# Kernel tuning notes

Hardware: AMD Instinct MI355X
Metric: run time of the kernel (lower is better)

Reference implementation:

```python
import jax, jax.numpy as jnp
import numpy as np

N, E, DN, DE, H, L = 2048, 32768, 512, 512, 8, 2
BN_EPS = 1e-5  # torch BatchNorm1d eps; eval mode with running_mean=0, running_var=1


def setup_inputs():
    key = jax.random.key(0)
    ks = jax.random.split(key, 12)
    rng = np.random.default_rng(0)
    # unique directed edges: 3E/4 upper-triangular pairs + reverses of the first E/4
    iu, ju = np.triu_indices(N, k=1)
    sel = rng.choice(iu.size, size=3 * E // 4, replace=False)
    s, d = iu[sel], ju[sel]
    src = np.concatenate([s, d[: E // 4]])
    dst = np.concatenate([d, s[: E // 4]])
    edge_index = jnp.asarray(np.stack([src, dst]).astype(np.int32))

    def p(k, shape, fan_in):
        return jax.random.normal(k, shape, jnp.float32) / np.sqrt(fan_in).astype(np.float32)

    return dict(
        x=jax.random.normal(ks[0], (N, DN), jnp.float32),
        edge_feature=jax.random.normal(ks[1], (E, DE), jnp.float32),
        node_pos=jax.random.uniform(ks[2], (N, 3), jnp.float32) * 10.0,
        inw=p(ks[3], (L, 3 * DN, DN), DN),          # MHA in_proj_weight per layer
        inb=jnp.zeros((L, 3 * DN), jnp.float32),
        ow=p(ks[4], (L, DN, DN), DN),               # MHA out_proj
        ob=jnp.zeros((L, DN), jnp.float32),
        etw=p(ks[5], (L, DE, DE), DE),              # edge_transform Linear
        etb=jnp.zeros((L, DE), jnp.float32),
        etg=jnp.ones((L, DE), jnp.float32),         # edge_transform BN gamma
        etbb=jnp.zeros((L, DE), jnp.float32),       # edge_transform BN beta
        unw=p(ks[6], (L, DN, DN + DE), DN + DE),    # update_node Linear
        unb=jnp.zeros((L, DN), jnp.float32),
        uew=p(ks[7], (L, DE, 2 * DN + 2 * DE), 2 * DN + 2 * DE),  # update_edge Linear
        ueb=jnp.zeros((L, DE), jnp.float32),
        edge_index=edge_index,
    )


def _forward(x, edge_feature, node_pos, inw, inb, ow, ob, etw, etb, etg, etbb, unw, unb, uew, ueb, edge_index):
    src, dst = edge_index[0], edge_index[1]
    n, e = x.shape[0], src.shape[0]
    hd = DN // H
    # vectorized reverse-edge lookup (mirrors the torch edge_dict)
    keys = src * n + dst
    rkeys = dst * n + src
    order = jnp.argsort(keys)
    sk = keys[order]
    pos = jnp.clip(jnp.searchsorted(sk, rkeys), 0, e - 1)
    found = sk[pos] == rkeys
    rev_idx = order[pos]
    # distance-based attention mask: -inf everywhere, 1/(dist+eps) on (symmetric) edges, 1.0 on diagonal
    diff = node_pos[src] - node_pos[dst]
    w = 1.0 / (jnp.sqrt(jnp.sum(diff * diff, axis=-1)) + 1e-6)
    mask = jnp.full((n, n), -jnp.inf, x.dtype)
    mask = mask.at[src, dst].set(w).at[dst, src].set(w)
    diag = jnp.arange(n)
    mask = mask.at[diag, diag].set(1.0)
    bn_scale = np.float32(1.0 / np.sqrt(1.0 + BN_EPS))
    nf, ef = x, edge_feature
    for l in range(L):
        rev = jnp.where(found[:, None], ef[rev_idx], 0.0)
        # MHSA over all nodes as one sequence (batch=1), eval mode (dropout off)
        qkv = nf @ inw[l].T + inb[l]
        q, k, v = [t.reshape(n, H, hd) for t in jnp.split(qkv, 3, axis=-1)]
        scores = jnp.einsum('nhd,mhd->hnm', q * np.float32(1.0 / np.sqrt(hd)), k) + mask
        attn = jax.nn.softmax(scores, axis=-1)
        ctx = jnp.einsum('hnm,mhd->nhd', attn, v).reshape(n, DN)
        x_upd = ctx @ ow[l].T + ob[l]
        # message: update_edge on [x_i, e, e_rev, x_j] (flow=target_to_source -> x_i = x[src])
        upd_edge = jnp.concatenate([nf[src], ef, rev, nf[dst]], axis=1) @ uew[l].T + ueb[l]
        # edge_transform = Linear + BN(eval) + ReLU
        te = jax.nn.relu((ef @ etw[l].T + etb[l]) * bn_scale * etg[l] + etbb[l])
        # scatter-max to subject/object nodes (empty segments -> 0, torch_scatter convention)
        subj = jax.ops.segment_max(te, src, num_segments=n)
        obj = jax.ops.segment_max(te, dst, num_segments=n)
        subj = jnp.where(jnp.isneginf(subj), 0.0, subj)
        obj = jnp.where(jnp.isneginf(obj), 0.0, obj)
        nf = jnp.concatenate([x_upd, subj + obj], axis=1) @ unw[l].T + unb[l]
        ef = upd_edge
        if l < L - 1 or L == 1:
            nf = jax.nn.relu(nf)
            ef = jax.nn.relu(ef)
    return nf, ef


def reference(x, edge_feature, node_pos, inw, inb, ow, ob, etw, etb, etg, etbb, unw, unb, uew, ueb, edge_index):
    return _forward(x, edge_feature, node_pos, inw, inb, ow, ob, etw, etb, etg, etbb, unw, unb, uew, ueb, edge_index)
```

## Files before the change

kernel.cpp:

```cpp
#include <hip/hip_runtime.h>
#include <hip/hip_bf16.h>

#define NN 2048
#define EE 32768
#define DND 512
#define NH 8
#define HD 64
#define MAXD 128
#define NEGF (-1e30f)
#define BN_SCALE 0.9999950000374997f

typedef __attribute__((ext_vector_type(8))) short bf16x8;
typedef __attribute__((ext_vector_type(4))) float f32x4;
typedef unsigned short u16;
typedef unsigned int u32;

static __device__ __forceinline__ float4 ld4(const float* p) {
    return *reinterpret_cast<const float4*>(p);
}
static __device__ __forceinline__ u16 f2b(float f) {
    __hip_bfloat16 h = __float2bfloat16(f);
    return *reinterpret_cast<u16*>(&h);
}
static __device__ __forceinline__ float b2f(u32 bits) {
    return __uint_as_float(bits << 16);
}
static __device__ __forceinline__ void gl_lds(const u16* g, u16* l) {
    __builtin_amdgcn_global_load_lds((const __attribute__((address_space(1))) void*)g,
                                     (__attribute__((address_space(3))) void*)l, 16, 0, 0);
}


__global__ __launch_bounds__(256) void setup_init_k(u32* __restrict__ t2,
                                                    int* __restrict__ adj, float* __restrict__ wadj,
                                                    int* __restrict__ cnt,
                                                    int* __restrict__ ocnt, int* __restrict__ icnt,
                                                    u16* __restrict__ zero)
{
    int i = blockIdx.x * 256 + threadIdx.x;
    t2[i] = 0xFFFFFFFFu;
    if (i < NN) {
        cnt[i] = 1; adj[i * MAXD] = i; wadj[i * MAXD] = 1.0f;
        ocnt[i] = 0; icnt[i] = 0;
    }
    if (i < 1024) zero[i] = 0;
}

__global__ __launch_bounds__(256) void fill_scatter_k(const int* __restrict__ ei, u16* __restrict__ t,
                                                      int* __restrict__ oadj, int* __restrict__ ocnt,
                                                      int* __restrict__ iadj, int* __restrict__ icnt)
{
    int e = blockIdx.x * 256 + threadIdx.x;
    if (e >= EE) return;
    int s = ei[e], d = ei[EE + e];
    t[(size_t)s * NN + d] = (u16)e;
    int slot = atomicAdd(&ocnt[s], 1);
    if (slot < MAXD) oadj[s * MAXD + slot] = e;
    slot = atomicAdd(&icnt[d], 1);
    if (slot < MAXD) iadj[d * MAXD + slot] = e;
}

__global__ __launch_bounds__(256) void rev_csr_k(const int* __restrict__ ei, const u16* __restrict__ t,
                                                 const float* __restrict__ pos,
                                                 int* __restrict__ rev,
                                                 int* __restrict__ adj, float* __restrict__ wadj,
                                                 int* __restrict__ cnt)
{
    int e = blockIdx.x * 256 + threadIdx.x;
    if (e >= EE) return;
    int s = ei[e], d = ei[EE + e];
    u16 r16 = t[(size_t)d * NN + s];
    int r = (r16 == 0xFFFFu) ? -1 : (int)r16;
    rev[e] = r;
    float dx = pos[s * 3 + 0] - pos[d * 3 + 0];
    float dy = pos[s * 3 + 1] - pos[d * 3 + 1];
    float dz = pos[s * 3 + 2] - pos[d * 3 + 2];
    float w = 1.0f / (sqrtf(dx * dx + dy * dy + dz * dz) + 1e-6f);
    int slot = atomicAdd(&cnt[s], 1);
    if (slot < MAXD) { adj[s * MAXD + slot] = d; wadj[s * MAXD + slot] = w; }
    if (r < 0) {
        slot = atomicAdd(&cnt[d], 1);
        if (slot < MAXD) { adj[d * MAXD + slot] = s; wadj[d * MAXD + slot] = w; }
    }
}

__global__ __launch_bounds__(256) void conv_all_k(
    const float* __restrict__ x, const float* __restrict__ inw, const float* __restrict__ ow,
    const float* __restrict__ etw, const float* __restrict__ unw, const float* __restrict__ uew,
    const float* __restrict__ efin, u16* __restrict__ dst)
{
    size_t i = ((size_t)blockIdx.x * 256 + threadIdx.x) * 8;
    const float* s;
    size_t off;
    if (i < 1048576)      { s = x;    off = i; }
    else if (i < 2621440) { s = inw;  off = i - 1048576; }
    else if (i < 3145728) { s = ow;   off = i - 2621440; }
    else if (i < 3670016) { s = etw;  off = i - 3145728; }
    else if (i < 4718592) { s = unw;  off = i - 3670016; }
    else if (i < 6815744) { s = uew;  off = i - 4718592; }
    else                  { s = efin; off = i - 6815744; }
    float4 a = ld4(s + off), b = ld4(s + off + 4);
    u16 o[8];
    o[0] = f2b(a.x); o[1] = f2b(a.y); o[2] = f2b(a.z); o[3] = f2b(a.w);
    o[4] = f2b(b.x); o[5] = f2b(b.y); o[6] = f2b(b.z); o[7] = f2b(b.w);
    *reinterpret_cast<int4*>(dst + i) = *reinterpret_cast<const int4*>(o);
}

__global__ __launch_bounds__(256) void gather_max_k(const u16* __restrict__ te,
                                                    const int* __restrict__ oadj, const int* __restrict__ ocnt,
                                                    const int* __restrict__ iadj, const int* __restrict__ icnt,
                                                    u16* __restrict__ sums)
{
    const int i = blockIdx.x;
    const int c2 = threadIdx.x;
    float ms0 = 0.f, ms1 = 0.f, mo0 = 0.f, mo1 = 0.f;
    int no = ocnt[i]; if (no > MAXD) no = MAXD;
    for (int s = 0; s < no; ++s) {
        const int e = oadj[i * MAXD + s];
        const u32 v = *reinterpret_cast<const u32*>(te + (size_t)e * DND + c2 * 2);
        ms0 = fmaxf(ms0, b2f(v & 0xffffu));
        ms1 = fmaxf(ms1, b2f(v >> 16));
    }
    int ni = icnt[i]; if (ni > MAXD) ni = MAXD;
    for (int s = 0; s < ni; ++s) {
        const int e = iadj[i * MAXD + s];
        const u32 v = *reinterpret_cast<const u32*>(te + (size_t)e * DND + c2 * 2);
        mo0 = fmaxf(mo0, b2f(v & 0xffffu));
        mo1 = fmaxf(mo1, b2f(v >> 16));
    }
    const u32 r = (u32)f2b(ms0 + mo0) | ((u32)f2b(ms1 + mo1) << 16);
    *reinterpret_cast<u32*>(sums + (size_t)i * DND + c2 * 2) = r;
}

template <int MODE, int EPI, int WF32, int WBF16, int GY>
__global__ __launch_bounds__(256) void mgemm_k(
    const u16* __restrict__ WS, u32 a_off, u32 b_off, const float* __restrict__ bias,
    float* __restrict__ Cf, u16* __restrict__ Cb, int M, int Nc, int K,
    u32 g0_off, u32 g1_off, u32 gz_off,
    const int* __restrict__ srcv, const int* __restrict__ dstv, const int* __restrict__ revv,
    const float* __restrict__ eg, const float* __restrict__ eb)
{
    __shared__ u16 As2[2][8192];
    __shared__ u16 Bs2[2][8192];
    const int tid = threadIdx.x, lane = tid & 63, w = tid >> 6;
    const int wr = w >> 1, wc = w & 1;
    const int b = blockIdx.x;
    const int xcd = b & 7, kb = b >> 3;
    const int bm = ((kb / GY) * 8 + xcd) * 128;
    const int bn = (kb % GY) * 128;

    const int rl = lane >> 3;
    const u32 lx = (u32)(((lane & 7) ^ rl) * 8);

    u32 offA0[4], offA1[4], offB[4];
#pragma unroll
    for (int q = 0; q < 4; ++q) {
        const int ra = bm + w * 32 + q * 8 + rl;
        if (MODE == 0) {
            offA0[q] = a_off + (u32)ra * (u32)K + lx;
        } else {
            offA0[q] = g0_off + (u32)ra * 512u + lx;
            offA1[q] = g1_off + (u32)ra * 512u + lx;
        }
        offB[q] = b_off + (u32)(bn + w * 32 + q * 8 + rl) * (u32)K + lx;
    }

    const int nks = K >> 6;
    const int kq = lane >> 4, li = lane & 15;

    auto stage = [&](int t, int buf) {
        const u32 k0 = (u32)t * 64u;
        const int seg = (MODE == 0) ? 0 : (int)(k0 >> 9);
#pragma unroll
        for (int q = 0; q < 4; ++q) {
            u32 oa = (MODE == 0) ? offA0[q] : (seg == 0 ? offA0[q] : offA1[q]);
            const u32 koff = (MODE == 0) ? k0 : (k0 & 511u);
            gl_lds(WS + oa + koff, &As2[buf][(w * 32 + q * 8) * 64]);
        }
#pragma unroll
        for (int q = 0; q < 4; ++q)
            gl_lds(WS + offB[q] + k0, &Bs2[buf][(w * 32 + q * 8) * 64]);
    };

    f32x4 acc[4][4] = {};
    const int baseA = (wr * 64 + li) * 64 + ((kq ^ (li & 7)) * 8);
    const int baseB = (wc * 64 + li) * 64 + ((kq ^ (li & 7)) * 8);

    stage(0, 0);
    for (int t = 0; t < nks; ++t) {
        const int cur = t & 1;
        if (t + 1 < nks) stage(t + 1, cur ^ 1);
        if (t + 1 < nks) asm volatile("s_waitcnt vmcnt(8)" ::: "memory");
        else             asm volatile("s_waitcnt vmcnt(0)" ::: "memory");
        __builtin_amdgcn_s_barrier();
        __builtin_amdgcn_sched_barrier(0);
#pragma unroll
        for (int sub = 0; sub < 2; ++sub) {
            const int sx = sub << 5;
            bf16x8 af[4], bf[4];
#pragma unroll
            for (int m = 0; m < 4; ++m)
                af[m] = *reinterpret_cast<const bf16x8*>(&As2[cur][(baseA + m * 1024) ^ sx]);
#pragma unroll
            for (int n = 0; n < 4; ++n)
                bf[n] = *reinterpret_cast<const bf16x8*>(&Bs2[cur][(baseB + n * 1024) ^ sx]);
#pragma unroll
            for (int m = 0; m < 4; ++m)
#pragma unroll
                for (int n = 0; n < 4; ++n)
                    acc[m][n] = __builtin_amdgcn_mfma_f32_16x16x32_bf16(af[m], bf[n], acc[m][n], 0, 0, 0);
        }
        __builtin_amdgcn_s_barrier();
        __builtin_amdgcn_sched_barrier(0);
    }

    float bsv[4], scv[4], shv[4];
#pragma unroll
    for (int n = 0; n < 4; ++n) {
        const int col = bn + wc * 64 + n * 16 + li;
        bsv[n] = bias[col];
        if (EPI == 2) { scv[n] = BN_SCALE * eg[col]; shv[n] = eb[col]; }
    }
#pragma unroll
    for (int m = 0; m < 4; ++m) {
#pragma unroll
        for (int n = 0; n < 4; ++n) {
            const int col = bn + wc * 64 + n * 16 + li;
#pragma unroll
            for (int i = 0; i < 4; ++i) {
                float v = acc[m][n][i] + bsv[n];
                if (EPI == 2) v = fmaxf(fmaf(v, scv[n], shv[n]), 0.f);
                else if (EPI == 1) v = fmaxf(v, 0.f);
                const int r = bm + wr * 64 + m * 16 + (lane >> 4) * 4 + i;
                if (WF32) Cf[(size_t)r * Nc + col] = v;
                if (WBF16) Cb[(size_t)r * Nc + col] = f2b(v);
            }
        }
    }
}

template <int MODE, int EPI, int WF32, int WBF16>
__global__ __launch_bounds__(512, 2) void mgemm256_k(
    const u16* __restrict__ WS, u32 a_off, u32 b_off, const float* __restrict__ bias,
    float* __restrict__ Cf, u16* __restrict__ Cb, int M, int Nc, int K,
    u32 g0_off, u32 g1_off, u32 gz_off,
    const int* __restrict__ srcv, const int* __restrict__ dstv, const int* __restrict__ revv,
    const float* __restrict__ eg, const float* __restrict__ eb)
{
    __shared__ u16 SB[65536];
    const int tid = threadIdx.x, lane = tid & 63, w = tid >> 6;
    const int wr = w >> 2, wc = w & 3;
    const int b = blockIdx.x;
    const int bm = ((b & 7) + 8 * (b >> 4)) * 256;
    const int bn = ((b >> 3) & 1) * 256;

    const int rl = lane >> 3;
    const u32 lx = (u32)(((lane & 7) ^ rl) * 8);

    u32 offA0[4], offA1[4], offA2[4], offA3[4], offB[4];
#pragma unroll
    for (int q = 0; q < 4; ++q) {
        const int ra = bm + w * 32 + q * 8 + rl;
        if (MODE == 0) {
            offA0[q] = a_off + (u32)ra * (u32)K + lx;
        } else {
            offA0[q] = g0_off + (u32)srcv[ra] * 512u + lx;
            offA1[q] = g1_off + (u32)ra * 512u + lx;
            const int rv = revv[ra];
            offA2[q] = (rv >= 0 ? g1_off + (u32)rv * 512u : gz_off) + lx;
            offA3[q] = g0_off + (u32)dstv[ra] * 512u + lx;
        }
        offB[q] = b_off + (u32)(bn + w * 32 + q * 8 + rl) * (u32)K + lx;
    }

    const int nks = K >> 6;
    const int kq = lane >> 4, li = lane & 15;

    auto stageA2 = [&](int t, int buf, int q0) {
        const u32 k0 = (u32)t * 64u;
        const int seg = (MODE == 0) ? 0 : (int)(k0 >> 9);
        const u32 koff = (MODE == 0) ? k0 : (k0 & 511u);
#pragma unroll
        for (int q = q0; q < q0 + 2; ++q) {
            u32 oa;
            if (MODE == 0) oa = offA0[q];
            else           oa = (seg == 0 ? offA0[q] : seg == 1 ? offA1[q] : seg == 2 ? offA2[q] : offA3[q]);
            gl_lds(WS + oa + koff, &SB[buf * 16384 + (w * 32 + q * 8) * 64]);
        }
    };
    auto stageB2 = [&](int t, int buf, int q0) {
        const u32 k0 = (u32)t * 64u;
#pragma unroll
        for (int q = q0; q < q0 + 2; ++q)
            gl_lds(WS + offB[q] + k0, &SB[32768 + buf * 16384 + (w * 32 + q * 8) * 64]);
    };

    f32x4 acc[8][4] = {};
    const int baseA = (wr * 128 + li) * 64 + ((kq ^ (li & 7)) * 8);
    const int baseB = (wc * 64 + li) * 64 + ((kq ^ (li & 7)) * 8);

    stageA2(0, 0, 0); stageA2(0, 0, 2); stageB2(0, 0, 0); stageB2(0, 0, 2);
    for (int t = 0; t < nks; ++t) {
        const int cur = t & 1;
        const bool pf = (t + 1 < nks);
        if (pf) {
            stageA2(t + 1, cur ^ 1, 0);
            asm volatile("s_waitcnt vmcnt(2)" ::: "memory");
        } else {
            asm volatile("s_waitcnt vmcnt(0)" ::: "memory");
        }
        __builtin_amdgcn_s_barrier();
        __builtin_amdgcn_sched_barrier(0);
#pragma unroll
        for (int sub = 0; sub < 2; ++sub) {
            const int sx = sub << 5;
            bf16x8 bf[4];
#pragma unroll
            for (int n = 0; n < 4; ++n)
                bf[n] = *reinterpret_cast<const bf16x8*>(&SB[(32768 + cur * 16384 + baseB + n * 1024) ^ sx]);
#pragma unroll
            for (int mh = 0; mh < 2; ++mh) {
                if (pf) {
                    if (sub == 0 && mh == 0)      stageA2(t + 1, cur ^ 1, 2);
                    else if (sub == 0 && mh == 1) stageB2(t + 1, cur ^ 1, 0);
                    else if (sub == 1 && mh == 0) stageB2(t + 1, cur ^ 1, 2);
                }
                bf16x8 af[4];
#pragma unroll
                for (int m = 0; m < 4; ++m)
                    af[m] = *reinterpret_cast<const bf16x8*>(&SB[(cur * 16384 + baseA + (mh * 4 + m) * 1024) ^ sx]);
                __builtin_amdgcn_sched_barrier(0);
                __builtin_amdgcn_s_setprio(1);
#pragma unroll
                for (int m = 0; m < 4; ++m)
#pragma unroll
                    for (int n = 0; n < 4; ++n)
                        acc[mh * 4 + m][n] =
                            __builtin_amdgcn_mfma_f32_16x16x32_bf16(af[m], bf[n], acc[mh * 4 + m][n], 0, 0, 0);
                __builtin_amdgcn_s_setprio(0);
                __builtin_amdgcn_sched_barrier(0);
            }
        }
        __builtin_amdgcn_s_barrier();
        __builtin_amdgcn_sched_barrier(0);
    }

    float bsv[4], scv[4], shv[4];
#pragma unroll
    for (int n = 0; n < 4; ++n) {
        const int col = bn + wc * 64 + n * 16 + li;
        bsv[n] = bias[col];
        if (EPI == 2) { scv[n] = BN_SCALE * eg[col]; shv[n] = eb[col]; }
    }
#pragma unroll
    for (int m = 0; m < 8; ++m) {
#pragma unroll
        for (int n = 0; n < 4; ++n) {
            const int col = bn + wc * 64 + n * 16 + li;
#pragma unroll
            for (int i = 0; i < 4; ++i) {
                float v = acc[m][n][i] + bsv[n];
                if (EPI == 2) v = fmaxf(fmaf(v, scv[n], shv[n]), 0.f);
                else if (EPI == 1) v = fmaxf(v, 0.f);
                const int r = bm + wr * 128 + m * 16 + (lane >> 4) * 4 + i;
                if (WF32) Cf[(size_t)r * Nc + col] = v;
                if (WBF16) Cb[(size_t)r * Nc + col] = f2b(v);
            }
        }
    }
}

__global__ __launch_bounds__(256) void attn_sp_k(const u16* __restrict__ qkvb,
                                                 const int* __restrict__ adj,
                                                 const float* __restrict__ wadj,
                                                 const int* __restrict__ cnt,
                                                 u16* __restrict__ ctxb)
{
    const int i = blockIdx.x;
    const int wv = threadIdx.x >> 6, lane = threadIdx.x & 63;
    const int h = blockIdx.y * 4 + wv;
    __shared__ float qs[4][64];
    qs[wv][lane] = b2f((u32)qkvb[(size_t)i * 1536 + h * HD + lane]) * 0.125f;
    __syncthreads();
    int deg = cnt[i];
    if (deg > MAXD) deg = MAXD;
    float m = -3.0e38f, lsum = 0.f, c = 0.f;
    for (int base = 0; base < deg; base += 64) {
        int nn_ = deg - base; if (nn_ > 64) nn_ = 64;
        int j = 0;
        float s = NEGF;
        if (lane < nn_) {
            j = adj[i * MAXD + base + lane];
            const float wgt = wadj[i * MAXD + base + lane];
            const u16* kr = qkvb + (size_t)j * 1536 + DND + h * HD;
            float accd = 0.f;
#pragma unroll
            for (int cq = 0; cq < 4; ++cq) {
                uint4 kv = *reinterpret_cast<const uint4*>(kr + cq * 16);
                const float* qp = &qs[wv][cq * 16];
                accd = fmaf(qp[0],  b2f(kv.x & 0xffffu), accd);
                accd = fmaf(qp[1],  b2f(kv.x >> 16), accd);
                accd = fmaf(qp[2],  b2f(kv.y & 0xffffu), accd);
                accd = fmaf(qp[3],  b2f(kv.y >> 16), accd);
                accd = fmaf(qp[4],  b2f(kv.z & 0xffffu), accd);
                accd = fmaf(qp[5],  b2f(kv.z >> 16), accd);
                accd = fmaf(qp[6],  b2f(kv.w & 0xffffu), accd);
                accd = fmaf(qp[7],  b2f(kv.w >> 16), accd);
                uint4 kv2 = *reinterpret_cast<const uint4*>(kr + cq * 16 + 8);
                accd = fmaf(qp[8],  b2f(kv2.x & 0xffffu), accd);
                accd = fmaf(qp[9],  b2f(kv2.x >> 16), accd);
                accd = fmaf(qp[10], b2f(kv2.y & 0xffffu), accd);
                accd = fmaf(qp[11], b2f(kv2.y >> 16), accd);
                accd = fmaf(qp[12], b2f(kv2.z & 0xffffu), accd);
                accd = fmaf(qp[13], b2f(kv2.z >> 16), accd);
                accd = fmaf(qp[14], b2f(kv2.w & 0xffffu), accd);
                accd = fmaf(qp[15], b2f(kv2.w >> 16), accd);
            }
            s = accd + wgt;
        }
        float mloc = s;
#pragma unroll
        for (int o = 1; o < 64; o <<= 1) mloc = fmaxf(mloc, __shfl_xor(mloc, o, 64));
        const float mnew = fmaxf(m, mloc);
        const float alpha = __expf(m - mnew);
        const float p = (lane < nn_) ? __expf(s - mnew) : 0.f;
        float ps = p;
#pragma unroll
        for (int o = 1; o < 64; o <<= 1) ps += __shfl_xor(ps, o, 64);
        lsum = lsum * alpha + ps;
        c *= alpha;
        for (int l = 0; l < nn_; ++l) {
            const float pj = __shfl(p, l, 64);
            const int jj = __shfl(j, l, 64);
            c = fmaf(pj, b2f((u32)qkvb[(size_t)jj * 1536 + 2 * DND + h * HD + lane]), c);
        }
        m = mnew;
    }
    ctxb[(size_t)i * DND + h * HD + lane] = f2b(c / lsum);
}

extern "C" void kernel_launch(void* const* d_in, const int* in_sizes, int n_in,
                              void* d_out, int out_size, void* d_ws, size_t ws_size,
                              hipStream_t stream)
{
    const float* x    = (const float*)d_in[0];
    const float* efin = (const float*)d_in[1];
    const float* pos  = (const float*)d_in[2];
    const float* inw  = (const float*)d_in[3];
    const float* inb  = (const float*)d_in[4];
    const float* ow   = (const float*)d_in[5];
    const float* ob   = (const float*)d_in[6];
    const float* etw  = (const float*)d_in[7];
    const float* etb  = (const float*)d_in[8];
    const float* etg  = (const float*)d_in[9];
    const float* etbb = (const float*)d_in[10];
    const float* unw  = (const float*)d_in[11];
    const float* unb  = (const float*)d_in[12];
    const float* uew  = (const float*)d_in[13];
    const float* ueb  = (const float*)d_in[14];
    const int*   ei   = (const int*)d_in[15];

    float* W = (float*)d_ws;
    u16*   qkvb  = (u16*)W;
    u16*   te    = (u16*)W;
    int*   rev   = (int*)(W + 8388608);
    u16*   zero  = (u16*)(W + 8421376);
    int*   adj   = (int*)(W + 8421888);
    float* wadj  = W + 8684032;
    int*   cnt   = (int*)(W + 8946176);
    int*   oadj  = (int*)(W + 8948224);
    int*   ocnt  = (int*)(W + 9210368);
    int*   iadj  = (int*)(W + 9212416);
    int*   icnt  = (int*)(W + 9474560);
    u16*   ctxb  = (u16*)(W + 9476608);
    u16*   xupdb = (u16*)(W + 10000896);
    u16*   sums  = (u16*)(W + 10525184);
    u16*   nfb   = (u16*)(W + 11049472);
    u16*   wbf   = (u16*)(W + 11573760);
    u16*   efbA  = (u16*)(W + 14457344);
    u16*   efbB  = (u16*)(W + 22845952);
    u16*   table = (u16*)efbA;

    u16* inwb = wbf;
    u16* owb  = wbf + 1572864;
    u16* etwb = wbf + 2097152;
    u16* unwb = wbf + 2621440;
    u16* uewb = wbf + 3670016;

    float* out_nf = (float*)d_out;
    float* out_ef = out_nf + (size_t)NN * DND;

    const int* srcv = ei;
    const int* dstv = ei + EE;

    const u16* WSu = (const u16*)d_ws;
    auto uoff = [&](const void* p) { return (u32)((const u16*)p - WSu); };

    setup_init_k<<<NN * NN / 512, 256, 0, stream>>>((u32*)table, adj, wadj, cnt, ocnt, icnt, zero);
    fill_scatter_k<<<EE / 256, 256, 0, stream>>>(ei, table, oadj, ocnt, iadj, icnt);
    rev_csr_k<<<EE / 256, 256, 0, stream>>>(ei, table, pos, rev, adj, wadj, cnt);
    conv_all_k<<<11520, 256, 0, stream>>>(x, inw, ow, etw, unw, uew, efin, nfb);

    for (int l = 0; l < 2; ++l) {
        const u16* efb_cur = l ? efbB : efbA;
        const u16* inwb_l = inwb + (size_t)l * 786432;
        const u16* owb_l  = owb  + (size_t)l * 262144;
        const u16* etwb_l = etwb + (size_t)l * 262144;
        const u16* unwb_l = unwb + (size_t)l * 524288;
        const u16* uewb_l = uewb + (size_t)l * 1048576;
        const float* inb_l  = inb  + (size_t)l * 1536;
        const float* ob_l   = ob   + (size_t)l * 512;
        const float* etb_l  = etb  + (size_t)l * 512;
        const float* etg_l  = etg  + (size_t)l * 512;
        const float* etbb_l = etbb + (size_t)l * 512;
        const float* unb_l  = unb  + (size_t)l * 512;
        const float* ueb_l  = ueb  + (size_t)l * 512;

        mgemm_k<0, 0, 0, 1, 12><<<192, 256, 0, stream>>>(
            WSu, uoff(nfb), uoff(inwb_l), inb_l, nullptr, qkvb, NN, 1536, DND,
            0, 0, 0, nullptr, nullptr, nullptr, nullptr, nullptr);

        attn_sp_k<<<dim3(NN, 2), 256, 0, stream>>>(qkvb, adj, wadj, cnt, ctxb);

        mgemm_k<0, 0, 0, 1, 4><<<64, 256, 0, stream>>>(
            WSu, uoff(ctxb), uoff(owb_l), ob_l, nullptr, xupdb, NN, DND, DND,
            0, 0, 0, nullptr, nullptr, nullptr, nullptr, nullptr);

        mgemm256_k<0, 2, 0, 1><<<256, 512, 0, stream>>>(
            WSu, uoff(efb_cur), uoff(etwb_l), etb_l, nullptr, te, EE, DND, DND,
            0, 0, 0, nullptr, nullptr, nullptr, etg_l, etbb_l);

        gather_max_k<<<NN, 256, 0, stream>>>(te, oadj, ocnt, iadj, icnt, sums);

        if (l == 0)
            mgemm256_k<1, 1, 0, 1><<<256, 512, 0, stream>>>(
                WSu, 0, uoff(uewb_l), ueb_l, nullptr, efbB, EE, DND, 2048,
                uoff(nfb), uoff(efb_cur), uoff(zero), srcv, dstv, rev, nullptr, nullptr);
        else
            mgemm256_k<1, 0, 1, 0><<<256, 512, 0, stream>>>(
                WSu, 0, uoff(uewb_l), ueb_l, out_ef, nullptr, EE, DND, 2048,
                uoff(nfb), uoff(efb_cur), uoff(zero), srcv, dstv, rev, nullptr, nullptr);

        if (l == 0)
            mgemm_k<2, 1, 0, 1, 4><<<64, 256, 0, stream>>>(
                WSu, 0, uoff(unwb_l), unb_l, nullptr, nfb, NN, DND, 1024,
                uoff(xupdb), uoff(sums), 0, nullptr, nullptr, nullptr, nullptr, nullptr);
        else
            mgemm_k<2, 0, 1, 0, 4><<<64, 256, 0, stream>>>(
                WSu, 0, uoff(unwb_l), unb_l, out_nf, nullptr, NN, DND, 1024,
                uoff(xupdb), uoff(sums), 0, nullptr, nullptr, nullptr, nullptr, nullptr);
    }
}
```

Measured before the change: 429.8 us.

## Restructure GEMM main loop into four-phase half-tile prefetch pipeline

Reorganizes the 256x256 bf16 MFMA GEMM main loop into four phases per K-step. Each phase loads an A/B quarter from LDS and issues a half-tile global-to-LDS prefetch up to two steps ahead, with staging rows remapped so each half-tile lands in a region that is no longer being read. The goal is to overlap global loads with MFMA work more deeply and to spread barriers across phases. In exchange it adds more barriers per K-step and intricate vmcnt accounting, which risks stalls or races if the counts are wrong.

```diff
diff --git a/kernel.cpp b/kernel.cpp
--- a/kernel.cpp
+++ b/kernel.cpp
@@ -257,92 +257,110 @@
     const int rl = lane >> 3;
     const u32 lx = (u32)(((lane & 7) ^ rl) * 8);
 
+    int arb[4], brb[4];
+#pragma unroll
+    for (int h = 0; h < 2; ++h)
+#pragma unroll
+        for (int q = 0; q < 2; ++q) {
+            arb[h * 2 + q] = (w < 4 ? w * 16 : 128 + (w - 4) * 16) + h * 64 + q * 8;
+            brb[h * 2 + q] = (w >> 1) * 64 + (w & 1) * 16 + h * 32 + q * 8;
+        }
+
     u32 offA0[4], offA1[4], offA2[4], offA3[4], offB[4];
 #pragma unroll
-    for (int q = 0; q < 4; ++q) {
-        const int ra = bm + w * 32 + q * 8 + rl;
+    for (int i = 0; i < 4; ++i) {
+        const int ra = bm + arb[i] + rl;
         if (MODE == 0) {
-            offA0[q] = a_off + (u32)ra * (u32)K + lx;
+            offA0[i] = a_off + (u32)ra * (u32)K + lx;
         } else {
-            offA0[q] = g0_off + (u32)srcv[ra] * 512u + lx;
-            offA1[q] = g1_off + (u32)ra * 512u + lx;
+            offA0[i] = g0_off + (u32)srcv[ra] * 512u + lx;
+            offA1[i] = g1_off + (u32)ra * 512u + lx;
             const int rv = revv[ra];
-            offA2[q] = (rv >= 0 ? g1_off + (u32)rv * 512u : gz_off) + lx;
-            offA3[q] = g0_off + (u32)dstv[ra] * 512u + lx;
-        }
-        offB[q] = b_off + (u32)(bn + w * 32 + q * 8 + rl) * (u32)K + lx;
+            offA2[i] = (rv >= 0 ? g1_off + (u32)rv * 512u : gz_off) + lx;
+            offA3[i] = g0_off + (u32)dstv[ra] * 512u + lx;
+        }
+        offB[i] = b_off + (u32)(bn + brb[i] + rl) * (u32)K + lx;
     }
 
     const int nks = K >> 6;
     const int kq = lane >> 4, li = lane & 15;
 
-    auto stageA2 = [&](int t, int buf, int q0) {
+    auto stageA = [&](int t, int h) {
         const u32 k0 = (u32)t * 64u;
+        const int par = t & 1;
         const int seg = (MODE == 0) ? 0 : (int)(k0 >> 9);
         const u32 koff = (MODE == 0) ? k0 : (k0 & 511u);
 #pragma unroll
-        for (int q = q0; q < q0 + 2; ++q) {
+        for (int q = 0; q < 2; ++q) {
+            const int i = h * 2 + q;
             u32 oa;
-            if (MODE == 0) oa = offA0[q];
-            else           oa = (seg == 0 ? offA0[q] : seg == 1 ? offA1[q] : seg == 2 ? offA2[q] : offA3[q]);
-            gl_lds(WS + oa + koff, &SB[buf * 16384 + (w * 32 + q * 8) * 64]);
+            if (MODE == 0) oa = offA0[i];
+            else           oa = (seg == 0 ? offA0[i] : seg == 1 ? offA1[i] : seg == 2 ? offA2[i] : offA3[i]);
+            gl_lds(WS + oa + koff, &SB[par * 16384 + arb[i] * 64]);
         }
     };
-    auto stageB2 = [&](int t, int buf, int q0) {
+    auto stageB = [&](int t, int h) {
         const u32 k0 = (u32)t * 64u;
-#pragma unroll
-        for (int q = q0; q < q0 + 2; ++q)
-            gl_lds(WS + offB[q] + k0, &SB[32768 + buf * 16384 + (w * 32 + q * 8) * 64]);
+        const int par = t & 1;
+#pragma unroll
+        for (int q = 0; q < 2; ++q) {
+            const int i = h * 2 + q;
+            gl_lds(WS + offB[i] + k0, &SB[32768 + par * 16384 + brb[i] * 64]);
+        }
     };
 
     f32x4 acc[8][4] = {};
-    const int baseA = (wr * 128 + li) * 64 + ((kq ^ (li & 7)) * 8);
-    const int baseB = (wc * 64 + li) * 64 + ((kq ^ (li & 7)) * 8);
-
-    stageA2(0, 0, 0); stageA2(0, 0, 2); stageB2(0, 0, 0); stageB2(0, 0, 2);
+    const u32 swz = (u32)((kq ^ (li & 7)) * 8);
+
+    stageA(0, 0); stageB(0, 0); stageA(0, 1); stageB(0, 1);
+    if (nks > 1) { stageA(1, 0); stageB(1, 0); }
+    asm volatile("s_waitcnt vmcnt(8)" ::: "memory");
+    __builtin_amdgcn_s_barrier();
+
     for (int t = 0; t < nks; ++t) {
-        const int cur = t & 1;
-        const bool pf = (t + 1 < nks);
-        if (pf) {
-            stageA2(t + 1, cur ^ 1, 0);
-            asm volatile("s_waitcnt vmcnt(2)" ::: "memory");
-        } else {
-            asm volatile("s_waitcnt vmcnt(0)" ::: "memory");
-        }
-        __builtin_amdgcn_s_barrier();
-        __builtin_amdgcn_sched_barrier(0);
-#pragma unroll
-        for (int sub = 0; sub < 2; ++sub) {
-            const int sx = sub << 5;
-            bf16x8 bf[4];
-#pragma unroll
-            for (int n = 0; n < 4; ++n)
-                bf[n] = *reinterpret_cast<const bf16x8*>(&SB[(32768 + cur * 16384 + baseB + n * 1024) ^ sx]);
-#pragma unroll
-            for (int mh = 0; mh < 2; ++mh) {
-                if (pf) {
-                    if (sub == 0 && mh == 0)      stageA2(t + 1, cur ^ 1, 2);
-                    else if (sub == 0 && mh == 1) stageB2(t + 1, cur ^ 1, 0);
-                    else if (sub == 1 && mh == 0) stageB2(t + 1, cur ^ 1, 2);
-                }
-                bf16x8 af[4];
-#pragma unroll
-                for (int m = 0; m < 4; ++m)
-                    af[m] = *reinterpret_cast<const bf16x8*>(&SB[(cur * 16384 + baseA + (mh * 4 + m) * 1024) ^ sx]);
-                __builtin_amdgcn_sched_barrier(0);
-                __builtin_amdgcn_s_setprio(1);
-#pragma unroll
-                for (int m = 0; m < 4; ++m)
-#pragma unroll
-                    for (int n = 0; n < 4; ++n)
-                        acc[mh * 4 + m][n] =
-                            __builtin_amdgcn_mfma_f32_16x16x32_bf16(af[m], bf[n], acc[mh * 4 + m][n], 0, 0, 0);
-                __builtin_amdgcn_s_setprio(0);
-                __builtin_amdgcn_sched_barrier(0);
+        const int pA = (t & 1) * 16384, pB = 32768 + (t & 1) * 16384;
+#pragma unroll
+        for (int ph = 0; ph < 4; ++ph) {
+            const int mq = ph >> 1, nq = ph & 1;
+            bf16x8 af[2][4], bf[2][2];
+#pragma unroll
+            for (int ks = 0; ks < 2; ++ks) {
+#pragma unroll
+                for (int mi = 0; mi < 4; ++mi)
+                    af[ks][mi] = *reinterpret_cast<const bf16x8*>(
+                        &SB[pA + (wr * 128 + (mq * 4 + mi) * 16 + li) * 64 + (swz ^ (ks << 5))]);
+#pragma unroll
+                for (int ni = 0; ni < 2; ++ni)
+                    bf[ks][ni] = *reinterpret_cast<const bf16x8*>(
+                        &SB[pB + (wc * 64 + (nq * 2 + ni) * 16 + li) * 64 + (swz ^ (ks << 5))]);
             }
-        }
-        __builtin_amdgcn_s_barrier();
-        __builtin_amdgcn_sched_barrier(0);
+            if (ph == 0)      { if (t + 1 < nks) stageA(t + 1, 1); }
+            else if (ph == 1) { if (t + 1 < nks) stageB(t + 1, 1); }
+            else if (ph == 2) { if (t + 2 < nks) stageA(t + 2, 0); }
+            else              { if (t + 2 < nks) stageB(t + 2, 0); }
+            __builtin_amdgcn_s_barrier();
+            asm volatile("s_waitcnt lgkmcnt(0)" ::: "memory");
+            __builtin_amdgcn_sched_barrier(0);
+            __builtin_amdgcn_s_setprio(1);
+#pragma unroll
+            for (int ks = 0; ks < 2; ++ks)
+#pragma unroll
+                for (int mi = 0; mi < 4; ++mi)
+#pragma unroll
+                    for (int ni = 0; ni < 2; ++ni)
+                        acc[mq * 4 + mi][nq * 2 + ni] = __builtin_amdgcn_mfma_f32_16x16x32_bf16(
+                            af[ks][mi], bf[ks][ni], acc[mq * 4 + mi][nq * 2 + ni], 0, 0, 0);
+            __builtin_amdgcn_s_setprio(0);
+            __builtin_amdgcn_sched_barrier(0);
+            if (ph == 0) {
+                if (t + 1 < nks) asm volatile("s_waitcnt vmcnt(6)" ::: "memory");
+                else             asm volatile("s_waitcnt vmcnt(0)" ::: "memory");
+            } else if (ph == 3) {
+                if (t + 2 < nks) asm volatile("s_waitcnt vmcnt(8)" ::: "memory");
+                else             asm volatile("s_waitcnt vmcnt(4)" ::: "memory");
+            }
+            __builtin_amdgcn_s_barrier();
+        }
     }
 
     float bsv[4], scv[4], shv[4];
```

Result: slower. 465.3 us (+8.3%).
